# Optimization experiments

Measured on AMD Instinct MI355X. Metric: run time of the kernel, lower is better.

The kernel has to match this reference:

```python
import jax, jax.numpy as jnp
import numpy as np

HIDDEN = 2048
HEADS = 16
HEAD_DIM = HIDDEN // HEADS
D_FF = 4 * HIDDEN
B, T = 2, 2048
LN_EPS = 1e-5


def setup_inputs() -> dict:
    key = jax.random.key(0)
    ks = jax.random.split(key, 12)
    s = 0.02
    x = jax.random.normal(ks[0], (B, T, HIDDEN), dtype=jnp.float32)
    # strict upper-triangular True == masked (causal)
    causal_mask = jnp.triu(jnp.ones((T, T), dtype=bool), k=1)
    # weights stored as [in, out] (equivalent to torch Linear weight.T)
    Wq = jax.random.normal(ks[1], (HIDDEN, HIDDEN), jnp.float32) * s
    Wk = jax.random.normal(ks[2], (HIDDEN, HIDDEN), jnp.float32) * s
    Wv = jax.random.normal(ks[3], (HIDDEN, HIDDEN), jnp.float32) * s
    Wo = jax.random.normal(ks[4], (HIDDEN, HIDDEN), jnp.float32) * s
    ln1_w = jnp.ones((HIDDEN,), jnp.float32)
    ln1_b = jnp.zeros((HIDDEN,), jnp.float32)
    ln2_w = jnp.ones((HIDDEN,), jnp.float32)
    ln2_b = jnp.zeros((HIDDEN,), jnp.float32)
    W1 = jax.random.normal(ks[5], (HIDDEN, D_FF), jnp.float32) * s
    b1 = jnp.zeros((D_FF,), jnp.float32)
    W2 = jax.random.normal(ks[6], (D_FF, HIDDEN), jnp.float32) * s
    b2 = jnp.zeros((HIDDEN,), jnp.float32)
    return dict(x=x, causal_mask=causal_mask, Wq=Wq, Wk=Wk, Wv=Wv, Wo=Wo,
                ln1_w=ln1_w, ln1_b=ln1_b, ln2_w=ln2_w, ln2_b=ln2_b,
                W1=W1, b1=b1, W2=W2, b2=b2)


def _layernorm(x, w, b):
    mu = jnp.mean(x, axis=-1, keepdims=True)
    var = jnp.mean(jnp.square(x - mu), axis=-1, keepdims=True)
    return (x - mu) * jax.lax.rsqrt(var + LN_EPS) * w + b


def reference(x, causal_mask, Wq, Wk, Wv, Wo, ln1_w, ln1_b, ln2_w, ln2_b, W1, b1, W2, b2):
    Bx, Tx, H = x.shape
    h = _layernorm(x, ln1_w, ln1_b)
    # [B, T, heads, head_dim] -> [B, heads, T, head_dim]
    q = (h @ Wq).reshape(Bx, Tx, HEADS, HEAD_DIM).transpose(0, 2, 1, 3)
    k = (h @ Wk).reshape(Bx, Tx, HEADS, HEAD_DIM).transpose(0, 2, 1, 3)
    v = (h @ Wv).reshape(Bx, Tx, HEADS, HEAD_DIM).transpose(0, 2, 1, 3)
    scale = 1.0 / jnp.sqrt(jnp.float32(HEAD_DIM))
    scores = jnp.einsum('bhqd,bhkd->bhqk', q, k) * scale  # [B, heads, T, T]
    scores = jnp.where(causal_mask, -jnp.inf, scores)
    attn = jax.nn.softmax(scores, axis=-1)
    out = jnp.einsum('bhqk,bhkd->bhqd', attn, v)  # [B, heads, T, head_dim]
    out = out.transpose(0, 2, 1, 3).reshape(Bx, Tx, H)
    x = x + out @ Wo
    h2 = _layernorm(x, ln2_w, ln2_b)
    mlp = jax.nn.silu(h2 @ W1 + b1) @ W2 + b2
    return x + mlp
```

## Files before the change

### kernel.cpp

```cpp
#include <hip/hip_runtime.h>

#define HID 2048
#define NH 16
#define DH 128
#define DFF 8192
#define BB 2
#define TT 2048
#define MROWS 4096

typedef __bf16 bf16x8 __attribute__((ext_vector_type(8)));
typedef __bf16 bf16x4 __attribute__((ext_vector_type(4)));
typedef float  f32x4  __attribute__((ext_vector_type(4)));

__device__ __forceinline__ f32x4 mfma16(bf16x8 a, bf16x8 b, f32x4 c) {
    return __builtin_amdgcn_mfma_f32_16x16x32_bf16(a, b, c, 0, 0, 0);
}

__device__ __forceinline__ void gload_lds16(const __bf16* gsrc, __bf16* ldst) {
    __builtin_amdgcn_global_load_lds(
        (const __attribute__((address_space(1))) void*)gsrc,
        (__attribute__((address_space(3))) void*)ldst, 16, 0, 0);
}

template<int K, int N>
__global__ __launch_bounds__(256) void transpose_bf16_kernel(
    const float* __restrict__ W, __bf16* __restrict__ Wt) {
    __shared__ float tile[64][65];
    int tx = threadIdx.x;
    int ty = threadIdx.y;
    int n0 = blockIdx.x * 64;
    int k0 = blockIdx.y * 64;
    #pragma unroll
    for (int i = 0; i < 16; i++) {
        int kk = ty * 16 + i;
        tile[tx][kk] = W[(size_t)(k0 + kk) * N + n0 + tx];
    }
    __syncthreads();
    #pragma unroll
    for (int i = 0; i < 16; i++) {
        int nn = ty * 16 + i;
        Wt[(size_t)(n0 + nn) * K + k0 + tx] = (__bf16)tile[nn][tx];
    }
}

__global__ __launch_bounds__(256) void ln_kernel(
    const float* __restrict__ x, const float* __restrict__ gw,
    const float* __restrict__ gb, __bf16* __restrict__ out) {
    int row = blockIdx.x;
    int t = threadIdx.x;
    const float* xr = x + (size_t)row * HID;
    float4 v0 = *(const float4*)(xr + t * 8);
    float4 v1 = *(const float4*)(xr + t * 8 + 4);
    float xv[8] = {v0.x, v0.y, v0.z, v0.w, v1.x, v1.y, v1.z, v1.w};
    float s = 0.f, q = 0.f;
    #pragma unroll
    for (int j = 0; j < 8; j++) { s += xv[j]; q += xv[j] * xv[j]; }
    #pragma unroll
    for (int off = 1; off < 64; off <<= 1) {
        s += __shfl_xor(s, off);
        q += __shfl_xor(q, off);
    }
    __shared__ float ssum[4], ssq[4];
    if ((t & 63) == 0) { ssum[t >> 6] = s; ssq[t >> 6] = q; }
    __syncthreads();
    s = ssum[0] + ssum[1] + ssum[2] + ssum[3];
    q = ssq[0] + ssq[1] + ssq[2] + ssq[3];
    float mu = s * (1.0f / HID);
    float var = q * (1.0f / HID) - mu * mu;
    float rs = rsqrtf(var + 1e-5f);
    bf16x8 o;
    #pragma unroll
    for (int j = 0; j < 8; j++)
        o[j] = (__bf16)((xv[j] - mu) * rs * gw[t * 8 + j] + gb[t * 8 + j]);
    *(bf16x8*)(out + (size_t)row * HID + t * 8) = o;
}

template<int EPI, int N, int K>
__global__ __launch_bounds__(256) void gemm_kernel(
    const __bf16* __restrict__ A, const __bf16* __restrict__ Bt,
    void* __restrict__ Cout, const float* __restrict__ resid,
    const float* __restrict__ bias) {
    __shared__ __align__(16) __bf16 As[128 * 32];
    __shared__ __align__(16) __bf16 Bs[128 * 32];
    int tid = threadIdx.x;
    int w = tid >> 6, l = tid & 63;
    int wr = w >> 1, wc = w & 1;
    int qi = l & 15, g = l >> 4;
    int row0 = blockIdx.y * 128, col0 = blockIdx.x * 128;

    f32x4 acc[4][4] = {};

    const __bf16* Abase = A + (size_t)(row0 + w * 32 + (l >> 2)) * K + (l & 3) * 8;
    const __bf16* Bbase = Bt + (size_t)(col0 + w * 32 + (l >> 2)) * K + (l & 3) * 8;

    for (int k0 = 0; k0 < K; k0 += 32) {
        __syncthreads();
        #pragma unroll
        for (int i = 0; i < 2; i++) {
            gload_lds16(Abase + (size_t)i * 16 * K + k0, As + (w * 2 + i) * 512);
            gload_lds16(Bbase + (size_t)i * 16 * K + k0, Bs + (w * 2 + i) * 512);
        }
        __syncthreads();
        bf16x8 af[4], bfr[4];
        #pragma unroll
        for (int m = 0; m < 4; m++)
            af[m] = *(const bf16x8*)(As + (wr * 64 + m * 16 + qi) * 32 + g * 8);
        #pragma unroll
        for (int n = 0; n < 4; n++)
            bfr[n] = *(const bf16x8*)(Bs + (wc * 64 + n * 16 + qi) * 32 + g * 8);
        #pragma unroll
        for (int m = 0; m < 4; m++)
            #pragma unroll
            for (int n = 0; n < 4; n++)
                acc[m][n] = mfma16(af[m], bfr[n], acc[m][n]);
    }

    #pragma unroll
    for (int m = 0; m < 4; m++) {
        #pragma unroll
        for (int n = 0; n < 4; n++) {
            int Rb = row0 + wr * 64 + m * 16 + g * 4;
            int C = col0 + wc * 64 + n * 16 + qi;
            if constexpr (EPI == 1) {
                bf16x4 pk;
                #pragma unroll
                for (int r = 0; r < 4; r++) pk[r] = (__bf16)acc[m][n][r];
                int b = Rb >> 11, t0 = Rb & 2047, hh = C >> 7, d = C & 127;
                *(bf16x4*)((__bf16*)Cout + ((size_t)(b * NH + hh) * DH + d) * TT + t0) = pk;
            } else {
                #pragma unroll
                for (int r = 0; r < 4; r++) {
                    int R = Rb + r;
                    float v = acc[m][n][r];
                    size_t idx = (size_t)R * N + C;
                    if constexpr (EPI == 0) {
                        ((__bf16*)Cout)[idx] = (__bf16)v;
                    } else if constexpr (EPI == 2) {
                        ((float*)Cout)[idx] = resid[idx] + v;
                    } else if constexpr (EPI == 3) {
                        float u = v + bias[C];
                        ((__bf16*)Cout)[idx] = (__bf16)(u / (1.f + __expf(-u)));
                    } else {
                        float u = v + bias[C];
                        ((float*)Cout)[idx] = resid[idx] + u;
                    }
                }
            }
        }
    }
}

__global__ __launch_bounds__(256) void attn_kernel(
    const __bf16* __restrict__ qh, const __bf16* __restrict__ kh,
    const __bf16* __restrict__ vt, __bf16* __restrict__ out) {
    __shared__ __align__(16) __bf16 Ks[64 * 128];
    __shared__ __align__(16) __bf16 Vts[128 * 64];
    __shared__ __align__(16) __bf16 plds[4][1024];
    int tid = threadIdx.x;
    int w = tid >> 6, l = tid & 63;
    int qi = l & 15, g = l >> 4;
    int bh = blockIdx.y;
    int b = bh >> 4, hd = bh & 15;
    int qtile = gridDim.x - 1 - blockIdx.x;
    int qbase = qtile * 64 + w * 16;
    int qg = qbase + qi;

    const __bf16* qrow = qh + ((size_t)b * TT + qg) * HID + hd * DH;
    const __bf16* kbase = kh + (size_t)b * TT * HID + hd * DH;
    const __bf16* vtb = vt + (size_t)bh * DH * TT;

    bf16x8 bq[4];
    #pragma unroll
    for (int kc = 0; kc < 4; kc++)
        bq[kc] = *(const bf16x8*)(qrow + kc * 32 + g * 8);

    f32x4 O[8] = {};
    float m_run = -3.0e38f, l_run = 0.f;
    const float scale = 0.08838834764831845f;
    int nt = qtile + 1;

    for (int it = 0; it < nt; it++) {
        int kv0 = it * 64;
        __syncthreads();
        #pragma unroll
        for (int i = 0; i < 4; i++) {
            int j = (w * 4 + i) * 64 + l;
            int r = j >> 4, u = j & 15;
            int cb = (u * 16) ^ ((r & 7) << 4);
            gload_lds16(kbase + (size_t)(kv0 + r) * HID + (cb >> 1),
                        Ks + (w * 4 + i) * 512);
        }
        #pragma unroll
        for (int i = 0; i < 4; i++) {
            int j = (w * 4 + i) * 64 + l;
            int r = j >> 3, u = j & 7;
            int cb = (u * 16) ^ ((r & 7) << 4);
            gload_lds16(vtb + (size_t)r * TT + kv0 + (cb >> 1),
                        Vts + (w * 4 + i) * 512);
        }
        __syncthreads();

        f32x4 st[4] = {};
        #pragma unroll
        for (int t = 0; t < 4; t++) {
            #pragma unroll
            for (int kc = 0; kc < 4; kc++) {
                int row = t * 16 + qi;
                int cb = (kc * 64 + g * 16) ^ ((qi & 7) << 4);
                bf16x8 ak = *(const bf16x8*)(Ks + row * 128 + (cb >> 1));
                st[t] = mfma16(ak, bq[kc], st[t]);
            }
        }
        float s[16];
        #pragma unroll
        for (int t = 0; t < 4; t++)
            #pragma unroll
            for (int r = 0; r < 4; r++) s[t * 4 + r] = st[t][r] * scale;
        #pragma unroll
        for (int i = 0; i < 16; i++) {
            int kvg = kv0 + (i >> 2) * 16 + g * 4 + (i & 3);
            if (kvg > qg) s[i] = -3.0e38f;
        }
        float mt = s[0];
        #pragma unroll
        for (int i = 1; i < 16; i++) mt = fmaxf(mt, s[i]);
        mt = fmaxf(mt, __shfl_xor(mt, 16));
        mt = fmaxf(mt, __shfl_xor(mt, 32));
        float m_new = fmaxf(m_run, mt);
        float alpha = __expf(m_run - m_new);
        float p[16], ps = 0.f;
        #pragma unroll
        for (int i = 0; i < 16; i++) { p[i] = __expf(s[i] - m_new); ps += p[i]; }
        ps += __shfl_xor(ps, 16);
        ps += __shfl_xor(ps, 32);
        l_run = l_run * alpha + ps;
        m_run = m_new;

        #pragma unroll
        for (int t = 0; t < 4; t++) {
            bf16x4 pk;
            #pragma unroll
            for (int r = 0; r < 4; r++) pk[r] = (__bf16)p[t * 4 + r];
            int cb = (t * 32 + g * 8) ^ ((qi & 7) << 4);
            *(bf16x4*)(&plds[w][qi * 64 + (cb >> 1)]) = pk;
        }

        float av[4];
        #pragma unroll
        for (int r = 0; r < 4; r++) av[r] = __shfl(alpha, (g << 4) | (g * 4 + r));
        #pragma unroll
        for (int oc = 0; oc < 8; oc++)
            #pragma unroll
            for (int r = 0; r < 4; r++) O[oc][r] *= av[r];

        #pragma unroll
        for (int h = 0; h < 2; h++) {
            int cbp = (h * 64 + g * 16) ^ ((qi & 7) << 4);
            bf16x8 ap = *(const bf16x8*)(&plds[w][qi * 64 + (cbp >> 1)]);
            #pragma unroll
            for (int oc = 0; oc < 8; oc++) {
                int row = oc * 16 + qi;
                int cb = (h * 64 + g * 16) ^ ((qi & 7) << 4);
                bf16x8 bv = *(const bf16x8*)(Vts + row * 64 + (cb >> 1));
                O[oc] = mfma16(ap, bv, O[oc]);
            }
        }
    }

    float linv[4];
    #pragma unroll
    for (int r = 0; r < 4; r++) {
        float lq = __shfl(l_run, (g << 4) | (g * 4 + r));
        linv[r] = 1.0f / lq;
    }
    __bf16* op = out + ((size_t)b * TT + qbase) * HID + hd * DH;
    #pragma unroll
    for (int oc = 0; oc < 8; oc++)
        #pragma unroll
        for (int r = 0; r < 4; r++)
            op[(size_t)(g * 4 + r) * HID + oc * 16 + qi] = (__bf16)(O[oc][r] * linv[r]);
}

extern "C" void kernel_launch(void* const* d_in, const int* in_sizes, int n_in,
                              void* d_out, int out_size, void* d_ws, size_t ws_size,
                              hipStream_t stream) {
    const float* x    = (const float*)d_in[0];
    const float* Wq   = (const float*)d_in[2];
    const float* Wk   = (const float*)d_in[3];
    const float* Wv   = (const float*)d_in[4];
    const float* Wo   = (const float*)d_in[5];
    const float* ln1w = (const float*)d_in[6];
    const float* ln1b = (const float*)d_in[7];
    const float* ln2w = (const float*)d_in[8];
    const float* ln2b = (const float*)d_in[9];
    const float* W1   = (const float*)d_in[10];
    const float* b1   = (const float*)d_in[11];
    const float* W2   = (const float*)d_in[12];
    const float* b2   = (const float*)d_in[13];
    float* outp = (float*)d_out;

    char* ws = (char*)d_ws;
    const size_t SZ_W   = (size_t)HID * HID * 2;
    const size_t SZ_WF  = (size_t)HID * DFF * 2;
    const size_t SZ_ACT = (size_t)MROWS * HID * 2;
    const size_t SZ_X32 = (size_t)MROWS * HID * 4;

    __bf16* wqT  = (__bf16*)(ws);
    __bf16* wkT  = (__bf16*)(ws + SZ_W);
    __bf16* wvT  = (__bf16*)(ws + 2 * SZ_W);
    __bf16* woT  = (__bf16*)(ws + 3 * SZ_W);
    __bf16* w1T  = (__bf16*)(ws + 4 * SZ_W);
    __bf16* w2T  = (__bf16*)(ws + 4 * SZ_W + SZ_WF);
    __bf16* h    = (__bf16*)(ws + 4 * SZ_W + 2 * SZ_WF);
    float*  x1   = (float*) (ws + 4 * SZ_W + 2 * SZ_WF + SZ_ACT);
    char*   base = ws + 4 * SZ_W + 2 * SZ_WF + SZ_ACT + SZ_X32;
    __bf16* qb   = (__bf16*)(base);
    __bf16* kb   = (__bf16*)(base + SZ_ACT);
    __bf16* vtb  = (__bf16*)(base + 2 * SZ_ACT);
    __bf16* attn = (__bf16*)(base + 3 * SZ_ACT);
    __bf16* mlp1 = (__bf16*)(base);

    dim3 blk256(256);
    transpose_bf16_kernel<HID, HID><<<dim3(32, 32), dim3(64, 4), 0, stream>>>(Wq, wqT);
    transpose_bf16_kernel<HID, HID><<<dim3(32, 32), dim3(64, 4), 0, stream>>>(Wk, wkT);
    transpose_bf16_kernel<HID, HID><<<dim3(32, 32), dim3(64, 4), 0, stream>>>(Wv, wvT);
    transpose_bf16_kernel<HID, HID><<<dim3(32, 32), dim3(64, 4), 0, stream>>>(Wo, woT);
    transpose_bf16_kernel<HID, DFF><<<dim3(128, 32), dim3(64, 4), 0, stream>>>(W1, w1T);
    transpose_bf16_kernel<DFF, HID><<<dim3(32, 128), dim3(64, 4), 0, stream>>>(W2, w2T);

    ln_kernel<<<MROWS, blk256, 0, stream>>>(x, ln1w, ln1b, h);

    gemm_kernel<0, HID, HID><<<dim3(16, 32), blk256, 0, stream>>>(h, wqT, qb, nullptr, nullptr);
    gemm_kernel<0, HID, HID><<<dim3(16, 32), blk256, 0, stream>>>(h, wkT, kb, nullptr, nullptr);
    gemm_kernel<1, HID, HID><<<dim3(16, 32), blk256, 0, stream>>>(h, wvT, vtb, nullptr, nullptr);

    attn_kernel<<<dim3(TT / 64, BB * NH), blk256, 0, stream>>>(qb, kb, vtb, attn);

    gemm_kernel<2, HID, HID><<<dim3(16, 32), blk256, 0, stream>>>(attn, woT, x1, x, nullptr);

    ln_kernel<<<MROWS, blk256, 0, stream>>>(x1, ln2w, ln2b, h);

    gemm_kernel<3, DFF, HID><<<dim3(64, 32), blk256, 0, stream>>>(h, w1T, mlp1, nullptr, b1);
    gemm_kernel<4, HID, DFF><<<dim3(16, 32), blk256, 0, stream>>>(mlp1, w2T, outp, x1, b2);
}
```

Baseline: 811.5 us.

## Replace GEMM with 256-row triple-buffered swizzled kernel and fuse QKV projections

The 128x128 GEMM with two barriers per k-step is replaced by a 512-thread kernel using 256-row tiles and a three-stage LDS ring filled by async global-to-LDS loads. It waits on explicit vmcnt counts, XOR-swizzles LDS addresses to avoid bank conflicts, raises wave priority around the MFMA block, and remaps workgroup IDs across eight groups. The Q, K and V projections become one GEMM over the contiguous transposed weights, with a split epilogue. The aim is more data reuse, overlap of loads with math, and fewer launches, at the cost of heavy LDS use that limits occupancy and fragile hand-written wait counts.

```diff
diff --git a/kernel.cpp b/kernel.cpp
--- a/kernel.cpp
+++ b/kernel.cpp
@@ -75,58 +75,133 @@
     *(bf16x8*)(out + (size_t)row * HID + t * 8) = o;
 }
 
-template<int EPI, int N, int K>
-__global__ __launch_bounds__(256) void gemm_kernel(
+template<int EPI, int BN, int BK, int N, int K>
+__global__ __launch_bounds__(512) void gemm8(
     const __bf16* __restrict__ A, const __bf16* __restrict__ Bt,
-    void* __restrict__ Cout, const float* __restrict__ resid,
-    const float* __restrict__ bias) {
-    __shared__ __align__(16) __bf16 As[128 * 32];
-    __shared__ __align__(16) __bf16 Bs[128 * 32];
+    void* __restrict__ C0, void* __restrict__ C1, void* __restrict__ C2,
+    const float* __restrict__ resid, const float* __restrict__ bias, int nN) {
+    constexpr int BM = 256;
+    constexpr int CPR = BK / 8;
+    constexpr int RND_A = BM * BK * 2 / 8192;
+    constexpr int RND_B = BN * BK * 2 / 8192;
+    constexpr int LPT = RND_A + RND_B;
+    constexpr int NT = K / BK;
+    constexpr int WC = BN / 4;
+    constexpr int NFRAG = WC / 16;
+    constexpr int KK = BK / 32;
+
+    __shared__ __align__(16) __bf16 As[3][BM * BK];
+    __shared__ __align__(16) __bf16 Bs[3][BN * BK];
+
     int tid = threadIdx.x;
     int w = tid >> 6, l = tid & 63;
-    int wr = w >> 1, wc = w & 1;
+    int wr = w >> 2, wc = w & 3;
     int qi = l & 15, g = l >> 4;
-    int row0 = blockIdx.y * 128, col0 = blockIdx.x * 128;
-
-    f32x4 acc[4][4] = {};
-
-    const __bf16* Abase = A + (size_t)(row0 + w * 32 + (l >> 2)) * K + (l & 3) * 8;
-    const __bf16* Bbase = Bt + (size_t)(col0 + w * 32 + (l >> 2)) * K + (l & 3) * 8;
-
-    for (int k0 = 0; k0 < K; k0 += 32) {
-        __syncthreads();
-        #pragma unroll
-        for (int i = 0; i < 2; i++) {
-            gload_lds16(Abase + (size_t)i * 16 * K + k0, As + (w * 2 + i) * 512);
-            gload_lds16(Bbase + (size_t)i * 16 * K + k0, Bs + (w * 2 + i) * 512);
-        }
-        __syncthreads();
-        bf16x8 af[4], bfr[4];
-        #pragma unroll
-        for (int m = 0; m < 4; m++)
-            af[m] = *(const bf16x8*)(As + (wr * 64 + m * 16 + qi) * 32 + g * 8);
-        #pragma unroll
-        for (int n = 0; n < 4; n++)
-            bfr[n] = *(const bf16x8*)(Bs + (wc * 64 + n * 16 + qi) * 32 + g * 8);
-        #pragma unroll
-        for (int m = 0; m < 4; m++)
-            #pragma unroll
-            for (int n = 0; n < 4; n++)
-                acc[m][n] = mfma16(af[m], bfr[n], acc[m][n]);
-    }
-
-    #pragma unroll
-    for (int m = 0; m < 4; m++) {
-        #pragma unroll
-        for (int n = 0; n < 4; n++) {
-            int Rb = row0 + wr * 64 + m * 16 + g * 4;
-            int C = col0 + wc * 64 + n * 16 + qi;
-            if constexpr (EPI == 1) {
-                bf16x4 pk;
+
+    int nwg = gridDim.x;
+    int bid = blockIdx.x;
+    int wg = (bid & 7) * (nwg >> 3) + (bid >> 3);
+    int bm = wg / nN, bn = wg % nN;
+    int row0 = bm * BM, col0 = bn * BN;
+
+    const __bf16* pA[RND_A];
+    #pragma unroll
+    for (int i = 0; i < RND_A; i++) {
+        int slot = i * 512 + tid;
+        int r = slot / CPR, u = slot % CPR;
+        pA[i] = A + (size_t)(row0 + r) * K + (u ^ (r & (CPR - 1))) * 8;
+    }
+    const __bf16* pB[RND_B];
+    #pragma unroll
+    for (int i = 0; i < RND_B; i++) {
+        int slot = i * 512 + tid;
+        int r = slot / CPR, u = slot % CPR;
+        pB[i] = Bt + (size_t)(col0 + r) * K + (u ^ (r & (CPR - 1))) * 8;
+    }
+    int wbase = w * 64 * 8;
+
+    f32x4 acc[8][NFRAG] = {};
+
+    #pragma unroll
+    for (int tt = 0; tt < 2; tt++) {
+        #pragma unroll
+        for (int i = 0; i < RND_A; i++)
+            gload_lds16(pA[i] + tt * BK, &As[tt][i * 4096 + wbase]);
+        #pragma unroll
+        for (int i = 0; i < RND_B; i++)
+            gload_lds16(pB[i] + tt * BK, &Bs[tt][i * 4096 + wbase]);
+    }
+
+    __bf16 *a0 = As[0], *a1 = As[1], *a2 = As[2];
+    __bf16 *b0 = Bs[0], *b1 = Bs[1], *b2 = Bs[2];
+
+    for (int t = 0; t < NT; t++) {
+        if constexpr (LPT == 6) asm volatile("s_waitcnt vmcnt(6)" ::: "memory");
+        else                    asm volatile("s_waitcnt vmcnt(4)" ::: "memory");
+        __builtin_amdgcn_s_barrier();
+        asm volatile("" ::: "memory");
+        if (t + 2 < NT) {
+            #pragma unroll
+            for (int i = 0; i < RND_A; i++)
+                gload_lds16(pA[i] + (t + 2) * BK, a2 + i * 4096 + wbase);
+            #pragma unroll
+            for (int i = 0; i < RND_B; i++)
+                gload_lds16(pB[i] + (t + 2) * BK, b2 + i * 4096 + wbase);
+        }
+        bf16x8 af[8][KK], bfr[NFRAG][KK];
+        #pragma unroll
+        for (int m = 0; m < 8; m++) {
+            int r = wr * 128 + m * 16 + qi;
+            #pragma unroll
+            for (int kk = 0; kk < KK; kk++) {
+                int byt = r * (BK * 2) + ((kk * 64 + g * 16) ^ ((r & (CPR - 1)) << 4));
+                af[m][kk] = *(const bf16x8*)((const char*)a0 + byt);
+            }
+        }
+        #pragma unroll
+        for (int n = 0; n < NFRAG; n++) {
+            int r = wc * WC + n * 16 + qi;
+            #pragma unroll
+            for (int kk = 0; kk < KK; kk++) {
+                int byt = r * (BK * 2) + ((kk * 64 + g * 16) ^ ((r & (CPR - 1)) << 4));
+                bfr[n][kk] = *(const bf16x8*)((const char*)b0 + byt);
+            }
+        }
+        __builtin_amdgcn_s_setprio(1);
+        #pragma unroll
+        for (int kk = 0; kk < KK; kk++)
+            #pragma unroll
+            for (int m = 0; m < 8; m++)
                 #pragma unroll
-                for (int r = 0; r < 4; r++) pk[r] = (__bf16)acc[m][n][r];
-                int b = Rb >> 11, t0 = Rb & 2047, hh = C >> 7, d = C & 127;
-                *(bf16x4*)((__bf16*)Cout + ((size_t)(b * NH + hh) * DH + d) * TT + t0) = pk;
+                for (int n = 0; n < NFRAG; n++)
+                    acc[m][n] = mfma16(af[m][kk], bfr[n][kk], acc[m][n]);
+        __builtin_amdgcn_s_setprio(0);
+        asm volatile("" ::: "memory");
+        __bf16* ta = a0; a0 = a1; a1 = a2; a2 = ta;
+        __bf16* tb = b0; b0 = b1; b1 = b2; b2 = tb;
+    }
+
+    #pragma unroll
+    for (int m = 0; m < 8; m++) {
+        #pragma unroll
+        for (int n = 0; n < NFRAG; n++) {
+            int Rb = row0 + wr * 128 + m * 16 + g * 4;
+            int C = col0 + wc * WC + n * 16 + qi;
+            if constexpr (EPI == 6) {
+                int region = C >> 11;
+                int Cl = C & 2047;
+                if (region < 2) {
+                    __bf16* dst = (__bf16*)(region == 0 ? C0 : C1);
+                    #pragma unroll
+                    for (int r = 0; r < 4; r++)
+                        dst[(size_t)(Rb + r) * 2048 + Cl] = (__bf16)acc[m][n][r];
+                } else {
+                    bf16x4 pk;
+                    #pragma unroll
+                    for (int r = 0; r < 4; r++) pk[r] = (__bf16)acc[m][n][r];
+                    int b = Rb >> 11, t0 = Rb & 2047, hh = Cl >> 7, d = Cl & 127;
+                    *(bf16x4*)((__bf16*)C2 + ((size_t)(b * NH + hh) * DH + d) * TT + t0) = pk;
+                }
             } else {
                 #pragma unroll
                 for (int r = 0; r < 4; r++) {
@@ -134,15 +209,15 @@
                     float v = acc[m][n][r];
                     size_t idx = (size_t)R * N + C;
                     if constexpr (EPI == 0) {
-                        ((__bf16*)Cout)[idx] = (__bf16)v;
+                        ((__bf16*)C0)[idx] = (__bf16)v;
                     } else if constexpr (EPI == 2) {
-                        ((float*)Cout)[idx] = resid[idx] + v;
+                        ((float*)C0)[idx] = resid[idx] + v;
                     } else if constexpr (EPI == 3) {
                         float u = v + bias[C];
-                        ((__bf16*)Cout)[idx] = (__bf16)(u / (1.f + __expf(-u)));
-                    } else {
+                        ((__bf16*)C0)[idx] = (__bf16)(u / (1.f + __expf(-u)));
+                    } else if constexpr (EPI == 4) {
                         float u = v + bias[C];
-                        ((float*)Cout)[idx] = resid[idx] + u;
+                        ((float*)C0)[idx] = resid[idx] + u;
                     }
                 }
             }
@@ -320,7 +395,7 @@
     __bf16* attn = (__bf16*)(base + 3 * SZ_ACT);
     __bf16* mlp1 = (__bf16*)(base);
 
-    dim3 blk256(256);
+    dim3 blk256(256), blk512(512);
     transpose_bf16_kernel<HID, HID><<<dim3(32, 32), dim3(64, 4), 0, stream>>>(Wq, wqT);
     transpose_bf16_kernel<HID, HID><<<dim3(32, 32), dim3(64, 4), 0, stream>>>(Wk, wkT);
     transpose_bf16_kernel<HID, HID><<<dim3(32, 32), dim3(64, 4), 0, stream>>>(Wv, wvT);
@@ -330,16 +405,18 @@
 
     ln_kernel<<<MROWS, blk256, 0, stream>>>(x, ln1w, ln1b, h);
 
-    gemm_kernel<0, HID, HID><<<dim3(16, 32), blk256, 0, stream>>>(h, wqT, qb, nullptr, nullptr);
-    gemm_kernel<0, HID, HID><<<dim3(16, 32), blk256, 0, stream>>>(h, wkT, kb, nullptr, nullptr);
-    gemm_kernel<1, HID, HID><<<dim3(16, 32), blk256, 0, stream>>>(h, wvT, vtb, nullptr, nullptr);
+    gemm8<6, 128, 64, 6144, HID><<<768, blk512, 0, stream>>>(
+        h, wqT, qb, kb, vtb, nullptr, nullptr, 48);
 
     attn_kernel<<<dim3(TT / 64, BB * NH), blk256, 0, stream>>>(qb, kb, vtb, attn);
 
-    gemm_kernel<2, HID, HID><<<dim3(16, 32), blk256, 0, stream>>>(attn, woT, x1, x, nullptr);
+    gemm8<2, 128, 64, HID, HID><<<256, blk512, 0, stream>>>(
+        attn, woT, x1, nullptr, nullptr, x, nullptr, 16);
 
     ln_kernel<<<MROWS, blk256, 0, stream>>>(x1, ln2w, ln2b, h);
 
-    gemm_kernel<3, DFF, HID><<<dim3(64, 32), blk256, 0, stream>>>(h, w1T, mlp1, nullptr, b1);
-    gemm_kernel<4, HID, DFF><<<dim3(16, 32), blk256, 0, stream>>>(mlp1, w2T, outp, x1, b2);
-}
+    gemm8<3, 256, 32, DFF, HID><<<512, blk512, 0, stream>>>(
+        h, w1T, mlp1, nullptr, nullptr, nullptr, b1, 32);
+    gemm8<4, 128, 64, HID, DFF><<<256, blk512, 0, stream>>>(
+        mlp1, w2T, outp, nullptr, nullptr, x1, b2, 16);
+}
```

After: 765.7 us. -5.6%, faster.

## Replace GEMMs with 256x256 double-buffered swizzled kernel, fused QKV, split-K MLP2

Applied to the files above, without the earlier changes.

Replaces the 128x128 single-buffered GEMM with a 512-thread 256x256 tile kernel. It uses a BK=64 double-buffered LDS pipeline with XOR-swizzled layout, interleaved staging, setprio and block-index remapping. The Q/K/V projections become one GEMM over a concatenated 6144-column weight, which relies on the three transposed weights sitting contiguously in the workspace. The final MLP GEMM uses split-K=2 with atomic adds onto an output pre-initialised with residual plus bias. Together these aim to raise data reuse, overlap loads with MFMA and fill the device, at the cost of atomic traffic and large LDS use per block.

```diff
diff --git a/kernel.cpp b/kernel.cpp
--- a/kernel.cpp
+++ b/kernel.cpp
@@ -75,74 +75,175 @@
     *(bf16x8*)(out + (size_t)row * HID + t * 8) = o;
 }
 
-template<int EPI, int N, int K>
-__global__ __launch_bounds__(256) void gemm_kernel(
+__global__ __launch_bounds__(256) void init_out_kernel(
+    const float* __restrict__ x1, const float* __restrict__ b2,
+    float* __restrict__ out) {
+    int i = blockIdx.x * 256 + threadIdx.x;
+    float4 a = ((const float4*)x1)[i];
+    float4 bb = ((const float4*)b2)[i & (HID / 4 - 1)];
+    float4 o = {a.x + bb.x, a.y + bb.y, a.z + bb.z, a.w + bb.w};
+    ((float4*)out)[i] = o;
+}
+
+template<int EPI, int KSPLIT, int N, int K>
+__global__ __launch_bounds__(512, 2) void gemm256(
     const __bf16* __restrict__ A, const __bf16* __restrict__ Bt,
-    void* __restrict__ Cout, const float* __restrict__ resid,
-    const float* __restrict__ bias) {
-    __shared__ __align__(16) __bf16 As[128 * 32];
-    __shared__ __align__(16) __bf16 Bs[128 * 32];
+    void* __restrict__ C0, void* __restrict__ C1, void* __restrict__ C2,
+    const float* __restrict__ resid, const float* __restrict__ bias, int nN) {
+    constexpr int BK = 64;
+    constexpr int KS = K / KSPLIT;
+    constexpr int NT = KS / BK;
+
+    __shared__ __align__(16) __bf16 As[2][16384];
+    __shared__ __align__(16) __bf16 Bs[2][16384];
+
     int tid = threadIdx.x;
     int w = tid >> 6, l = tid & 63;
-    int wr = w >> 1, wc = w & 1;
+    int wm = w >> 2, wn = w & 3;
     int qi = l & 15, g = l >> 4;
-    int row0 = blockIdx.y * 128, col0 = blockIdx.x * 128;
-
-    f32x4 acc[4][4] = {};
-
-    const __bf16* Abase = A + (size_t)(row0 + w * 32 + (l >> 2)) * K + (l & 3) * 8;
-    const __bf16* Bbase = Bt + (size_t)(col0 + w * 32 + (l >> 2)) * K + (l & 3) * 8;
-
-    for (int k0 = 0; k0 < K; k0 += 32) {
-        __syncthreads();
+
+    int nwg = gridDim.x;
+    int bid = blockIdx.x;
+    int wg = (bid & 7) * (nwg >> 3) + (bid >> 3);
+    int nMN = nwg / KSPLIT;
+    int tileid = wg % nMN;
+    int kh = wg / nMN;
+    int bm = tileid / nN, bn = tileid % nN;
+    int row0 = bm * 256, col0 = bn * 256;
+    int kb0 = kh * KS;
+
+    int offA[2][2], offB[2][2];
+    #pragma unroll
+    for (int h = 0; h < 2; h++)
         #pragma unroll
         for (int i = 0; i < 2; i++) {
-            gload_lds16(Abase + (size_t)i * 16 * K + k0, As + (w * 2 + i) * 512);
-            gload_lds16(Bbase + (size_t)i * 16 * K + k0, Bs + (w * 2 + i) * 512);
-        }
-        __syncthreads();
-        bf16x8 af[4], bfr[4];
-        #pragma unroll
-        for (int m = 0; m < 4; m++)
-            af[m] = *(const bf16x8*)(As + (wr * 64 + m * 16 + qi) * 32 + g * 8);
-        #pragma unroll
-        for (int n = 0; n < 4; n++)
-            bfr[n] = *(const bf16x8*)(Bs + (wc * 64 + n * 16 + qi) * 32 + g * 8);
-        #pragma unroll
-        for (int m = 0; m < 4; m++)
-            #pragma unroll
-            for (int n = 0; n < 4; n++)
-                acc[m][n] = mfma16(af[m], bfr[n], acc[m][n]);
-    }
-
-    #pragma unroll
-    for (int m = 0; m < 4; m++) {
-        #pragma unroll
-        for (int n = 0; n < 4; n++) {
-            int Rb = row0 + wr * 64 + m * 16 + g * 4;
-            int C = col0 + wc * 64 + n * 16 + qi;
-            if constexpr (EPI == 1) {
-                bf16x4 pk;
-                #pragma unroll
-                for (int r = 0; r < 4; r++) pk[r] = (__bf16)acc[m][n][r];
-                int b = Rb >> 11, t0 = Rb & 2047, hh = C >> 7, d = C & 127;
-                *(bf16x4*)((__bf16*)Cout + ((size_t)(b * NH + hh) * DH + d) * TT + t0) = pk;
+            int slot = i * 512 + tid;
+            int r = slot >> 3, u8 = slot & 7;
+            offA[h][i] = (row0 + h * 128 + r) * K + kb0 + (u8 ^ (r & 7)) * 8;
+            offB[h][i] = (col0 + h * 128 + r) * K + kb0 + (u8 ^ (r & 7)) * 8;
+        }
+    int dstoff = w * 512;
+
+    f32x4 acc[8][4] = {};
+    bf16x8 aF[4][2], bF0[2][2], bF1[2][2];
+
+    auto stageA = [&](int u, int h) {
+        #pragma unroll
+        for (int i = 0; i < 2; i++)
+            gload_lds16(A + offA[h][i] + u * BK,
+                        &As[u & 1][h * 8192 + i * 4096 + dstoff]);
+    };
+    auto stageB = [&](int u, int h) {
+        #pragma unroll
+        for (int i = 0; i < 2; i++)
+            gload_lds16(Bt + offB[h][i] + u * BK,
+                        &Bs[u & 1][h * 8192 + i * 4096 + dstoff]);
+    };
+    auto loadA = [&](int s, int qm) {
+        #pragma unroll
+        for (int mi = 0; mi < 4; mi++) {
+            int rA = qm * 128 + wm * 64 + mi * 16 + qi;
+            #pragma unroll
+            for (int kk = 0; kk < 2; kk++) {
+                int byt = rA * 128 + ((kk * 64 + g * 16) ^ ((rA & 7) << 4));
+                aF[mi][kk] = *(const bf16x8*)((const char*)As[s] + byt);
+            }
+        }
+    };
+    auto loadB = [&](bf16x8 (&bF)[2][2], int s, int qn) {
+        #pragma unroll
+        for (int ni = 0; ni < 2; ni++) {
+            int rB = qn * 128 + wn * 32 + ni * 16 + qi;
+            #pragma unroll
+            for (int kk = 0; kk < 2; kk++) {
+                int byt = rB * 128 + ((kk * 64 + g * 16) ^ ((rB & 7) << 4));
+                bF[ni][kk] = *(const bf16x8*)((const char*)Bs[s] + byt);
+            }
+        }
+    };
+
+    #define MMAC(BF, FMB, FNB)                                             \
+        asm volatile("s_waitcnt lgkmcnt(0)" ::: "memory");                 \
+        __builtin_amdgcn_sched_barrier(0);                                 \
+        __builtin_amdgcn_s_setprio(1);                                     \
+        _Pragma("unroll")                                                  \
+        for (int kk = 0; kk < 2; kk++)                                     \
+            _Pragma("unroll")                                              \
+            for (int mi = 0; mi < 4; mi++)                                 \
+                _Pragma("unroll")                                          \
+                for (int ni = 0; ni < 2; ni++)                             \
+                    acc[(FMB) + mi][(FNB) + ni] =                          \
+                        mfma16(aF[mi][kk], BF[ni][kk],                     \
+                               acc[(FMB) + mi][(FNB) + ni]);               \
+        __builtin_amdgcn_s_setprio(0);
+
+    stageA(0, 0); stageB(0, 0); stageA(0, 1); stageB(0, 1);
+    if (NT > 1) { stageA(1, 0); stageB(1, 0); stageA(1, 1); }
+    asm volatile("s_waitcnt vmcnt(6)" ::: "memory");
+    __builtin_amdgcn_s_barrier();
+
+    for (int t = 0; t < NT; t++) {
+        int s = t & 1;
+        loadA(s, 0); loadB(bF0, s, 0);
+        if (t + 1 < NT) stageB(t + 1, 1);
+        __builtin_amdgcn_s_barrier();
+        MMAC(bF0, 0, 0)
+        __builtin_amdgcn_s_barrier();
+        loadB(bF1, s, 1);
+        if (t + 2 < NT) stageA(t + 2, 0);
+        __builtin_amdgcn_s_barrier();
+        MMAC(bF1, 0, 2)
+        __builtin_amdgcn_s_barrier();
+        loadA(s, 1);
+        if (t + 2 < NT) stageB(t + 2, 0);
+        __builtin_amdgcn_s_barrier();
+        MMAC(bF0, 4, 0)
+        __builtin_amdgcn_s_barrier();
+        if (t + 2 < NT) stageA(t + 2, 1);
+        __builtin_amdgcn_s_barrier();
+        MMAC(bF1, 4, 2)
+        if (t + 2 < NT)      asm volatile("s_waitcnt vmcnt(6)" ::: "memory");
+        else if (t + 1 < NT) asm volatile("s_waitcnt vmcnt(0)" ::: "memory");
+        __builtin_amdgcn_s_barrier();
+    }
+    #undef MMAC
+
+    #pragma unroll
+    for (int fm = 0; fm < 8; fm++) {
+        int qm = fm >> 2, mi = fm & 3;
+        int Rb = row0 + qm * 128 + wm * 64 + mi * 16 + g * 4;
+        #pragma unroll
+        for (int fn = 0; fn < 4; fn++) {
+            int qn = fn >> 1, ni = fn & 1;
+            int C = col0 + qn * 128 + wn * 32 + ni * 16 + qi;
+            f32x4 v = acc[fm][fn];
+            if constexpr (EPI == 6) {
+                int region = C >> 11;
+                int Cl = C & 2047;
+                if (region < 2) {
+                    __bf16* dst = (__bf16*)(region == 0 ? C0 : C1);
+                    #pragma unroll
+                    for (int r = 0; r < 4; r++)
+                        dst[(size_t)(Rb + r) * 2048 + Cl] = (__bf16)v[r];
+                } else {
+                    bf16x4 pk;
+                    #pragma unroll
+                    for (int r = 0; r < 4; r++) pk[r] = (__bf16)v[r];
+                    int b = Rb >> 11, t0 = Rb & 2047, hh = Cl >> 7, d = Cl & 127;
+                    *(bf16x4*)((__bf16*)C2 +
+                        ((size_t)(b * NH + hh) * DH + d) * TT + t0) = pk;
+                }
             } else {
                 #pragma unroll
                 for (int r = 0; r < 4; r++) {
-                    int R = Rb + r;
-                    float v = acc[m][n][r];
-                    size_t idx = (size_t)R * N + C;
-                    if constexpr (EPI == 0) {
-                        ((__bf16*)Cout)[idx] = (__bf16)v;
-                    } else if constexpr (EPI == 2) {
-                        ((float*)Cout)[idx] = resid[idx] + v;
+                    size_t idx = (size_t)(Rb + r) * N + C;
+                    if constexpr (EPI == 2) {
+                        ((float*)C0)[idx] = resid[idx] + v[r];
                     } else if constexpr (EPI == 3) {
-                        float u = v + bias[C];
-                        ((__bf16*)Cout)[idx] = (__bf16)(u / (1.f + __expf(-u)));
-                    } else {
-                        float u = v + bias[C];
-                        ((float*)Cout)[idx] = resid[idx] + u;
+                        float u = v[r] + bias[C];
+                        ((__bf16*)C0)[idx] = (__bf16)(u / (1.f + __expf(-u)));
+                    } else if constexpr (EPI == 5) {
+                        atomicAdd((float*)C0 + idx, v[r]);
                     }
                 }
             }
@@ -320,7 +421,7 @@
     __bf16* attn = (__bf16*)(base + 3 * SZ_ACT);
     __bf16* mlp1 = (__bf16*)(base);
 
-    dim3 blk256(256);
+    dim3 blk256(256), blk512(512);
     transpose_bf16_kernel<HID, HID><<<dim3(32, 32), dim3(64, 4), 0, stream>>>(Wq, wqT);
     transpose_bf16_kernel<HID, HID><<<dim3(32, 32), dim3(64, 4), 0, stream>>>(Wk, wkT);
     transpose_bf16_kernel<HID, HID><<<dim3(32, 32), dim3(64, 4), 0, stream>>>(Wv, wvT);
@@ -330,16 +431,20 @@
 
     ln_kernel<<<MROWS, blk256, 0, stream>>>(x, ln1w, ln1b, h);
 
-    gemm_kernel<0, HID, HID><<<dim3(16, 32), blk256, 0, stream>>>(h, wqT, qb, nullptr, nullptr);
-    gemm_kernel<0, HID, HID><<<dim3(16, 32), blk256, 0, stream>>>(h, wkT, kb, nullptr, nullptr);
-    gemm_kernel<1, HID, HID><<<dim3(16, 32), blk256, 0, stream>>>(h, wvT, vtb, nullptr, nullptr);
+    gemm256<6, 1, 6144, HID><<<384, blk512, 0, stream>>>(
+        h, wqT, qb, kb, vtb, nullptr, nullptr, 24);
 
     attn_kernel<<<dim3(TT / 64, BB * NH), blk256, 0, stream>>>(qb, kb, vtb, attn);
 
-    gemm_kernel<2, HID, HID><<<dim3(16, 32), blk256, 0, stream>>>(attn, woT, x1, x, nullptr);
+    gemm256<2, 1, HID, HID><<<128, blk512, 0, stream>>>(
+        attn, woT, x1, nullptr, nullptr, x, nullptr, 8);
 
     ln_kernel<<<MROWS, blk256, 0, stream>>>(x1, ln2w, ln2b, h);
 
-    gemm_kernel<3, DFF, HID><<<dim3(64, 32), blk256, 0, stream>>>(h, w1T, mlp1, nullptr, b1);
-    gemm_kernel<4, HID, DFF><<<dim3(16, 32), blk256, 0, stream>>>(mlp1, w2T, outp, x1, b2);
-}
+    gemm256<3, 1, DFF, HID><<<512, blk512, 0, stream>>>(
+        h, w1T, mlp1, nullptr, nullptr, nullptr, b1, 32);
+
+    init_out_kernel<<<MROWS * HID / 4 / 256, blk256, 0, stream>>>(x1, b2, outp);
+    gemm256<5, 2, HID, DFF><<<256, blk512, 0, stream>>>(
+        mlp1, w2T, outp, nullptr, nullptr, nullptr, nullptr, 8);
+}
```

Result: faster. 788.5 us (-2.8%).

## Restructure GEMMs: BK64 swizzled LDS, fused QKV, split-K atomics, XCD remap

Applied to the files above, without the earlier changes.

Replaces the GEMM kernel with a BK=64 variant. Its LDS layout is XOR-swizzled to avoid bank conflicts, and tile ids are remapped across XCDs for better cache locality. The Q, K and V projections become one wide GEMM over the contiguous transposed weights, with the epilogue routing each column region to its output. The Wo and W2 GEMMs use split-K with float atomicAdd onto outputs pre-initialized with residual and bias. The weight transpose is also vectorized with float4 loads and bf16x4 stores. Atomics add an extra init pass and make the summation order nondeterministic.

```diff
diff --git a/kernel.cpp b/kernel.cpp
--- a/kernel.cpp
+++ b/kernel.cpp
@@ -26,20 +26,25 @@
 __global__ __launch_bounds__(256) void transpose_bf16_kernel(
     const float* __restrict__ W, __bf16* __restrict__ Wt) {
     __shared__ float tile[64][65];
-    int tx = threadIdx.x;
-    int ty = threadIdx.y;
-    int n0 = blockIdx.x * 64;
-    int k0 = blockIdx.y * 64;
-    #pragma unroll
-    for (int i = 0; i < 16; i++) {
-        int kk = ty * 16 + i;
-        tile[tx][kk] = W[(size_t)(k0 + kk) * N + n0 + tx];
+    int t = threadIdx.x;
+    int n0 = blockIdx.x * 64, k0 = blockIdx.y * 64;
+    int n4 = (t & 15) * 4, kk = t >> 4;
+    #pragma unroll
+    for (int i = 0; i < 4; i++) {
+        int k = i * 16 + kk;
+        float4 v = *(const float4*)(W + (size_t)(k0 + k) * N + n0 + n4);
+        tile[k][n4] = v.x; tile[k][n4 + 1] = v.y;
+        tile[k][n4 + 2] = v.z; tile[k][n4 + 3] = v.w;
     }
     __syncthreads();
-    #pragma unroll
-    for (int i = 0; i < 16; i++) {
-        int nn = ty * 16 + i;
-        Wt[(size_t)(n0 + nn) * K + k0 + tx] = (__bf16)tile[nn][tx];
+    int k4 = (t & 15) * 4, nn = t >> 4;
+    #pragma unroll
+    for (int i = 0; i < 4; i++) {
+        int n = i * 16 + nn;
+        bf16x4 o;
+        #pragma unroll
+        for (int j = 0; j < 4; j++) o[j] = (__bf16)tile[k4 + j][n];
+        *(bf16x4*)(Wt + (size_t)(n0 + n) * K + k0 + k4) = o;
     }
 }
 
@@ -75,74 +80,124 @@
     *(bf16x8*)(out + (size_t)row * HID + t * 8) = o;
 }
 
-template<int EPI, int N, int K>
-__global__ __launch_bounds__(256) void gemm_kernel(
+template<int HB>
+__global__ __launch_bounds__(256) void init_resid_kernel(
+    const float* __restrict__ src, const float* __restrict__ bias,
+    float* __restrict__ out) {
+    int i = blockIdx.x * 256 + threadIdx.x;
+    float4 a = ((const float4*)src)[i];
+    if constexpr (HB) {
+        float4 bb = ((const float4*)bias)[i & (HID / 4 - 1)];
+        a.x += bb.x; a.y += bb.y; a.z += bb.z; a.w += bb.w;
+    }
+    ((float4*)out)[i] = a;
+}
+
+template<int EPI, int KSPLIT, int N, int K>
+__global__ __launch_bounds__(256) void gemm128(
     const __bf16* __restrict__ A, const __bf16* __restrict__ Bt,
-    void* __restrict__ Cout, const float* __restrict__ resid,
-    const float* __restrict__ bias) {
-    __shared__ __align__(16) __bf16 As[128 * 32];
-    __shared__ __align__(16) __bf16 Bs[128 * 32];
+    void* __restrict__ C0, void* __restrict__ C1, void* __restrict__ C2,
+    const float* __restrict__ resid, const float* __restrict__ bias, int nN) {
+    constexpr int BK = 64;
+    constexpr int KS = K / KSPLIT;
+    constexpr int NT = KS / BK;
+
+    __shared__ __align__(16) __bf16 As[128 * BK];
+    __shared__ __align__(16) __bf16 Bs[128 * BK];
+
     int tid = threadIdx.x;
     int w = tid >> 6, l = tid & 63;
     int wr = w >> 1, wc = w & 1;
     int qi = l & 15, g = l >> 4;
-    int row0 = blockIdx.y * 128, col0 = blockIdx.x * 128;
+
+    int nwg = gridDim.x, bid = blockIdx.x;
+    int wg = (bid & 7) * (nwg >> 3) + (bid >> 3);
+    int nMN = nwg / KSPLIT;
+    int tileid = wg % nMN, kh = wg / nMN;
+    int bm = tileid / nN, bn = tileid % nN;
+    int row0 = bm * 128, col0 = bn * 128, kb0 = kh * KS;
+
+    const __bf16 *pA[4], *pB[4];
+    __bf16 *dA[4], *dB[4];
+    #pragma unroll
+    for (int i = 0; i < 4; i++) {
+        int slot = i * 256 + tid;
+        int r = slot >> 3, u8 = slot & 7;
+        pA[i] = A + (size_t)(row0 + r) * K + kb0 + (u8 ^ (r & 7)) * 8;
+        pB[i] = Bt + (size_t)(col0 + r) * K + kb0 + (u8 ^ (r & 7)) * 8;
+        dA[i] = As + (i * 256 + w * 64) * 8;
+        dB[i] = Bs + (i * 256 + w * 64) * 8;
+    }
+
+    int xk0 = (g * 16) ^ ((qi & 7) << 4);
+    int xk1 = (64 + g * 16) ^ ((qi & 7) << 4);
+    const char* arow = (const char*)As + (wr * 64 + qi) * 128;
+    const char* brow = (const char*)Bs + (wc * 64 + qi) * 128;
 
     f32x4 acc[4][4] = {};
 
-    const __bf16* Abase = A + (size_t)(row0 + w * 32 + (l >> 2)) * K + (l & 3) * 8;
-    const __bf16* Bbase = Bt + (size_t)(col0 + w * 32 + (l >> 2)) * K + (l & 3) * 8;
-
-    for (int k0 = 0; k0 < K; k0 += 32) {
+    for (int t = 0; t < NT; t++) {
         __syncthreads();
         #pragma unroll
-        for (int i = 0; i < 2; i++) {
-            gload_lds16(Abase + (size_t)i * 16 * K + k0, As + (w * 2 + i) * 512);
-            gload_lds16(Bbase + (size_t)i * 16 * K + k0, Bs + (w * 2 + i) * 512);
-        }
+        for (int i = 0; i < 4; i++) gload_lds16(pA[i] + t * BK, dA[i]);
+        #pragma unroll
+        for (int i = 0; i < 4; i++) gload_lds16(pB[i] + t * BK, dB[i]);
         __syncthreads();
-        bf16x8 af[4], bfr[4];
-        #pragma unroll
-        for (int m = 0; m < 4; m++)
-            af[m] = *(const bf16x8*)(As + (wr * 64 + m * 16 + qi) * 32 + g * 8);
-        #pragma unroll
-        for (int n = 0; n < 4; n++)
-            bfr[n] = *(const bf16x8*)(Bs + (wc * 64 + n * 16 + qi) * 32 + g * 8);
-        #pragma unroll
-        for (int m = 0; m < 4; m++)
-            #pragma unroll
-            for (int n = 0; n < 4; n++)
-                acc[m][n] = mfma16(af[m], bfr[n], acc[m][n]);
+
+        bf16x8 aF[4][2], bF[4][2];
+        #pragma unroll
+        for (int m = 0; m < 4; m++) {
+            aF[m][0] = *(const bf16x8*)(arow + m * 2048 + xk0);
+            aF[m][1] = *(const bf16x8*)(arow + m * 2048 + xk1);
+        }
+        #pragma unroll
+        for (int n = 0; n < 4; n++) {
+            bF[n][0] = *(const bf16x8*)(brow + n * 2048 + xk0);
+            bF[n][1] = *(const bf16x8*)(brow + n * 2048 + xk1);
+        }
+        #pragma unroll
+        for (int kk = 0; kk < 2; kk++)
+            #pragma unroll
+            for (int m = 0; m < 4; m++)
+                #pragma unroll
+                for (int n = 0; n < 4; n++)
+                    acc[m][n] = mfma16(aF[m][kk], bF[n][kk], acc[m][n]);
     }
 
     #pragma unroll
     for (int m = 0; m < 4; m++) {
+        int Rb = row0 + wr * 64 + m * 16 + g * 4;
         #pragma unroll
         for (int n = 0; n < 4; n++) {
-            int Rb = row0 + wr * 64 + m * 16 + g * 4;
             int C = col0 + wc * 64 + n * 16 + qi;
-            if constexpr (EPI == 1) {
-                bf16x4 pk;
-                #pragma unroll
-                for (int r = 0; r < 4; r++) pk[r] = (__bf16)acc[m][n][r];
-                int b = Rb >> 11, t0 = Rb & 2047, hh = C >> 7, d = C & 127;
-                *(bf16x4*)((__bf16*)Cout + ((size_t)(b * NH + hh) * DH + d) * TT + t0) = pk;
+            f32x4 v = acc[m][n];
+            if constexpr (EPI == 6) {
+                int region = C >> 11;
+                int Cl = C & 2047;
+                if (region < 2) {
+                    __bf16* dst = (__bf16*)(region == 0 ? C0 : C1);
+                    #pragma unroll
+                    for (int r = 0; r < 4; r++)
+                        dst[(size_t)(Rb + r) * 2048 + Cl] = (__bf16)v[r];
+                } else {
+                    bf16x4 pk;
+                    #pragma unroll
+                    for (int r = 0; r < 4; r++) pk[r] = (__bf16)v[r];
+                    int b = Rb >> 11, t0 = Rb & 2047, hh = Cl >> 7, d = Cl & 127;
+                    *(bf16x4*)((__bf16*)C2 +
+                        ((size_t)(b * NH + hh) * DH + d) * TT + t0) = pk;
+                }
             } else {
                 #pragma unroll
                 for (int r = 0; r < 4; r++) {
-                    int R = Rb + r;
-                    float v = acc[m][n][r];
-                    size_t idx = (size_t)R * N + C;
-                    if constexpr (EPI == 0) {
-                        ((__bf16*)Cout)[idx] = (__bf16)v;
-                    } else if constexpr (EPI == 2) {
-                        ((float*)Cout)[idx] = resid[idx] + v;
+                    size_t idx = (size_t)(Rb + r) * N + C;
+                    if constexpr (EPI == 2) {
+                        ((float*)C0)[idx] = resid[idx] + v[r];
                     } else if constexpr (EPI == 3) {
-                        float u = v + bias[C];
-                        ((__bf16*)Cout)[idx] = (__bf16)(u / (1.f + __expf(-u)));
-                    } else {
-                        float u = v + bias[C];
-                        ((float*)Cout)[idx] = resid[idx] + u;
+                        float u = v[r] + bias[C];
+                        ((__bf16*)C0)[idx] = (__bf16)(u / (1.f + __expf(-u)));
+                    } else if constexpr (EPI == 5) {
+                        atomicAdd((float*)C0 + idx, v[r]);
                     }
                 }
             }
@@ -321,25 +376,30 @@
     __bf16* mlp1 = (__bf16*)(base);
 
     dim3 blk256(256);
-    transpose_bf16_kernel<HID, HID><<<dim3(32, 32), dim3(64, 4), 0, stream>>>(Wq, wqT);
-    transpose_bf16_kernel<HID, HID><<<dim3(32, 32), dim3(64, 4), 0, stream>>>(Wk, wkT);
-    transpose_bf16_kernel<HID, HID><<<dim3(32, 32), dim3(64, 4), 0, stream>>>(Wv, wvT);
-    transpose_bf16_kernel<HID, HID><<<dim3(32, 32), dim3(64, 4), 0, stream>>>(Wo, woT);
-    transpose_bf16_kernel<HID, DFF><<<dim3(128, 32), dim3(64, 4), 0, stream>>>(W1, w1T);
-    transpose_bf16_kernel<DFF, HID><<<dim3(32, 128), dim3(64, 4), 0, stream>>>(W2, w2T);
+    transpose_bf16_kernel<HID, HID><<<dim3(32, 32), blk256, 0, stream>>>(Wq, wqT);
+    transpose_bf16_kernel<HID, HID><<<dim3(32, 32), blk256, 0, stream>>>(Wk, wkT);
+    transpose_bf16_kernel<HID, HID><<<dim3(32, 32), blk256, 0, stream>>>(Wv, wvT);
+    transpose_bf16_kernel<HID, HID><<<dim3(32, 32), blk256, 0, stream>>>(Wo, woT);
+    transpose_bf16_kernel<HID, DFF><<<dim3(128, 32), blk256, 0, stream>>>(W1, w1T);
+    transpose_bf16_kernel<DFF, HID><<<dim3(32, 128), blk256, 0, stream>>>(W2, w2T);
 
     ln_kernel<<<MROWS, blk256, 0, stream>>>(x, ln1w, ln1b, h);
 
-    gemm_kernel<0, HID, HID><<<dim3(16, 32), blk256, 0, stream>>>(h, wqT, qb, nullptr, nullptr);
-    gemm_kernel<0, HID, HID><<<dim3(16, 32), blk256, 0, stream>>>(h, wkT, kb, nullptr, nullptr);
-    gemm_kernel<1, HID, HID><<<dim3(16, 32), blk256, 0, stream>>>(h, wvT, vtb, nullptr, nullptr);
+    gemm128<6, 1, 6144, HID><<<1536, blk256, 0, stream>>>(
+        h, wqT, qb, kb, vtb, nullptr, nullptr, 48);
 
     attn_kernel<<<dim3(TT / 64, BB * NH), blk256, 0, stream>>>(qb, kb, vtb, attn);
 
-    gemm_kernel<2, HID, HID><<<dim3(16, 32), blk256, 0, stream>>>(attn, woT, x1, x, nullptr);
+    init_resid_kernel<0><<<MROWS * HID / 4 / 256, blk256, 0, stream>>>(x, nullptr, x1);
+    gemm128<5, 2, HID, HID><<<1024, blk256, 0, stream>>>(
+        attn, woT, x1, nullptr, nullptr, nullptr, nullptr, 16);
 
     ln_kernel<<<MROWS, blk256, 0, stream>>>(x1, ln2w, ln2b, h);
 
-    gemm_kernel<3, DFF, HID><<<dim3(64, 32), blk256, 0, stream>>>(h, w1T, mlp1, nullptr, b1);
-    gemm_kernel<4, HID, DFF><<<dim3(16, 32), blk256, 0, stream>>>(mlp1, w2T, outp, x1, b2);
-}
+    gemm128<3, 1, DFF, HID><<<2048, blk256, 0, stream>>>(
+        h, w1T, mlp1, nullptr, nullptr, nullptr, b1, 64);
+
+    init_resid_kernel<1><<<MROWS * HID / 4 / 256, blk256, 0, stream>>>(x1, b2, outp);
+    gemm128<5, 2, HID, DFF><<<1024, blk256, 0, stream>>>(
+        mlp1, w2T, outp, nullptr, nullptr, nullptr, nullptr, 16);
+}
```

New measurement: 855.7 us. +5.4%, slower.
